# Performance work log

Hardware: AMD Instinct MI355X
Metric: run time of the kernel (lower is better)

The kernel has to match this reference:

```python
import jax, jax.numpy as jnp
import numpy as np

N, IN_F, OUT_F, R = 8192, 4096, 4096, 16
ALPHA = 32
SCALING = ALPHA / R  # 2.0


def setup_inputs() -> dict:
    key = jax.random.key(0)
    k1, k2, k3, k4, k5 = jax.random.split(key, 5)
    return {
        "x": jax.random.normal(k1, (N, IN_F), dtype=jnp.float32),
        "W": jax.random.normal(k2, (OUT_F, IN_F), dtype=jnp.float32) * 0.02,
        "b": jax.random.normal(k3, (OUT_F,), dtype=jnp.float32) * 0.02,
        "lora_A": jax.random.normal(k4, (R, IN_F), dtype=jnp.float32) * 0.02,
        "lora_B": jax.random.normal(k5, (OUT_F, R), dtype=jnp.float32) * 0.02,
    }


def reference(x, W, b, lora_A, lora_B):
    # Base linear: x [N, in_f] @ W.T [in_f, out_f] + b -> [N, out_f]
    result = jnp.einsum('ni,oi->no', x, W) + b
    # LoRA path: (B @ (A @ x.T)).T * scaling == (x @ A.T) @ B.T * scaling
    lora = jnp.einsum('nr,or->no', jnp.einsum('ni,ri->nr', x, lora_A), lora_B)
    return result + lora * SCALING
```

## Files before the change

kernel.cpp:

```cpp
#include <hip/hip_runtime.h>
#include <hip/hip_bf16.h>
#include <stdint.h>

#define N_ROWS 8192
#define IN_F   4096
#define OUT_F  4096
#define R_LORA 16
#define KP     4160

typedef __bf16 bf16_t;
typedef __attribute__((ext_vector_type(8))) __bf16 bf16x8;
typedef __attribute__((ext_vector_type(4))) __bf16 bf16x4;
typedef __attribute__((ext_vector_type(4))) float  f32x4;
typedef __attribute__((ext_vector_type(16))) float f32x16;

__device__ __forceinline__ void load16_lds(const bf16_t* g, bf16_t* l) {
    auto gp = (const __attribute__((address_space(1))) void*)g;
    auto lp = (__attribute__((address_space(3))) void*)(uint32_t)(uintptr_t)l;
    __builtin_amdgcn_global_load_lds(gp, lp, 16, 0, 0);
}

#define PREPA_BLOCKS 2048

__global__ __launch_bounds__(256) void prep_fused(const float* __restrict__ x,
                                                  const float* __restrict__ W,
                                                  const float* __restrict__ bias,
                                                  const float* __restrict__ lA,
                                                  const float* __restrict__ lB,
                                                  bf16_t* __restrict__ Aw,
                                                  bf16_t* __restrict__ Bw) {
    int b = blockIdx.x;
    int t = threadIdx.x;
    if (b < PREPA_BLOCKS) {
        int row0 = b * 4;
        for (int rr = 0; rr < 4; ++rr) {
            int row = row0 + rr;
            const float4* xr = (const float4*)(x + (size_t)row * IN_F);
            bf16_t* ar = Aw + (size_t)row * KP;
            for (int s = t; s < 512; s += 256) {
                float4 f0 = xr[2 * s];
                float4 f1 = xr[2 * s + 1];
                bf16x8 v;
                v[0] = (bf16_t)f0.x; v[1] = (bf16_t)f0.y;
                v[2] = (bf16_t)f0.z; v[3] = (bf16_t)f0.w;
                v[4] = (bf16_t)f1.x; v[5] = (bf16_t)f1.y;
                v[6] = (bf16_t)f1.z; v[7] = (bf16_t)f1.w;
                *(bf16x8*)(ar + s * 8) = v;
            }
            if (t < 64) ar[IN_F + t] = (t == 0) ? (bf16_t)1.0f : (bf16_t)0.0f;
        }
    } else {
        int o0 = (b - PREPA_BLOCKS) * 4;
        float bl[4][R_LORA];
        for (int oo = 0; oo < 4; ++oo)
            for (int r = 0; r < R_LORA; ++r)
                bl[oo][r] = 2.0f * lB[(o0 + oo) * R_LORA + r];

        for (int j = 0; j < IN_F / (256 * 4); ++j) {
            int i4 = (j * 256 + t) * 4;
            f32x4 acc[4];
            for (int oo = 0; oo < 4; ++oo) {
                float4 w = *(const float4*)(W + (size_t)(o0 + oo) * IN_F + i4);
                acc[oo] = (f32x4){w.x, w.y, w.z, w.w};
            }
            for (int r = 0; r < R_LORA; ++r) {
                float4 a = *(const float4*)(lA + (size_t)r * IN_F + i4);
                for (int oo = 0; oo < 4; ++oo) {
                    acc[oo][0] += bl[oo][r] * a.x;
                    acc[oo][1] += bl[oo][r] * a.y;
                    acc[oo][2] += bl[oo][r] * a.z;
                    acc[oo][3] += bl[oo][r] * a.w;
                }
            }
            for (int oo = 0; oo < 4; ++oo) {
                bf16x4 v;
                v[0] = (bf16_t)acc[oo][0]; v[1] = (bf16_t)acc[oo][1];
                v[2] = (bf16_t)acc[oo][2]; v[3] = (bf16_t)acc[oo][3];
                *(bf16x4*)(Bw + (size_t)(o0 + oo) * KP + i4) = v;
            }
        }
        {
            int oo = t >> 6;
            int c  = IN_F + (t & 63);
            float v = (c == IN_F) ? bias[o0 + oo] : 0.0f;
            Bw[(size_t)(o0 + oo) * KP + c] = (bf16_t)v;
        }
    }
}

#define BM 256
#define BN 256
#define BK 64
#define NT (KP / BK)

__global__ __launch_bounds__(512, 2) void gemm_bt(const bf16_t* __restrict__ A,
                                                  const bf16_t* __restrict__ B,
                                                  float* __restrict__ C) {
    __shared__ __align__(16) bf16_t lds[2][2][BM * BK];

    int bid = blockIdx.x;
    int swz = (bid & 7) * 64 + (bid >> 3);
    int bm  = swz & 31;
    int bn  = swz >> 5;
    int rowBase = bm * BM;
    int colBase = bn * BN;

    const int t    = threadIdx.x;
    const int lane = t & 63;
    const int wave = t >> 6;
    const int l31  = lane & 31;
    const int lhi  = lane >> 5;
    const int l7   = lane & 7;
    const int lsw  = l7 ^ (2 * (l31 >> 3));
    const int wr   = wave >> 2;
    const int wc   = wave & 3;

    int rowOffA[4], colOffB[2];
#pragma unroll
    for (int rf = 0; rf < 4; ++rf) rowOffA[rf] = (wr * 128 + rf * 32 + l31) * BK;
#pragma unroll
    for (int cf = 0; cf < 2; ++cf) colOffB[cf] = (wc * 64 + cf * 32 + l31) * BK;

    uint32_t srcA[4], srcB[4];
#pragma unroll
    for (int s = 0; s < 4; ++s) {
        int c = s * 512 + t;
        int r = c >> 3, p = c & 7;
        int ck = p ^ (r & 7) ^ (2 * ((r >> 3) & 3));
        uint32_t off = (uint32_t)(r * KP + (ck << 3));
        srcA[s] = (uint32_t)(rowBase * KP) + off;
        srcB[s] = (uint32_t)(colBase * KP) + off;
    }

    auto stage = [&](int bsel, int k0) {
#pragma unroll
        for (int s = 0; s < 4; ++s)
            load16_lds(A + srcA[s] + k0, &lds[bsel][0][(s * 512 + t) * 8]);
#pragma unroll
        for (int s = 0; s < 4; ++s)
            load16_lds(B + srcB[s] + k0, &lds[bsel][1][(s * 512 + t) * 8]);
    };

    f32x16 acc[4][2];
#pragma unroll
    for (int rf = 0; rf < 4; ++rf)
#pragma unroll
        for (int cf = 0; cf < 2; ++cf)
#pragma unroll
            for (int r = 0; r < 16; ++r) acc[rf][cf][r] = 0.f;

#define COMPUTE(bsel)                                                          \
    do {                                                                       \
        const bf16_t* Ab = &lds[bsel][0][0];                                   \
        const bf16_t* Bb = &lds[bsel][1][0];                                   \
        _Pragma("unroll")                                                      \
        for (int ks = 0; ks < 4; ++ks) {                                       \
            int pos = ((((ks << 1) | lhi)) ^ lsw) << 3;                        \
            bf16x8 af[4], bf[2];                                               \
            _Pragma("unroll")                                                  \
            for (int rf = 0; rf < 4; ++rf)                                     \
                af[rf] = *(const bf16x8*)&Ab[rowOffA[rf] + pos];               \
            _Pragma("unroll")                                                  \
            for (int cf = 0; cf < 2; ++cf)                                     \
                bf[cf] = *(const bf16x8*)&Bb[colOffB[cf] + pos];               \
            __builtin_amdgcn_s_setprio(1);                                     \
            _Pragma("unroll")                                                  \
            for (int rf = 0; rf < 4; ++rf)                                     \
                _Pragma("unroll")                                              \
                for (int cf = 0; cf < 2; ++cf)                                 \
                    acc[rf][cf] = __builtin_amdgcn_mfma_f32_32x32x16_bf16(     \
                        af[rf], bf[cf], acc[rf][cf], 0, 0, 0);                 \
            __builtin_amdgcn_s_setprio(0);                                     \
        }                                                                      \
    } while (0)

    stage(0, 0);

    for (int kt = 0; kt < NT - 1; ++kt) {
        const int cur = kt & 1;
        const int nb  = cur ^ 1;
        __builtin_amdgcn_s_barrier();
        stage(nb, (kt + 1) * BK);
        asm volatile("s_waitcnt vmcnt(8)" ::: "memory");
        __builtin_amdgcn_s_barrier();
        COMPUTE(cur);
    }
    {
        __builtin_amdgcn_s_barrier();
        asm volatile("s_waitcnt vmcnt(0)" ::: "memory");
        __builtin_amdgcn_s_barrier();
        COMPUTE(0);
    }
#undef COMPUTE

#pragma unroll
    for (int rf = 0; rf < 4; ++rf) {
        int rB = rowBase + wr * 128 + rf * 32 + 4 * lhi;
#pragma unroll
        for (int cf = 0; cf < 2; ++cf) {
            int col = colBase + wc * 64 + cf * 32 + l31;
#pragma unroll
            for (int reg = 0; reg < 16; ++reg) {
                int row = rB + (reg & 3) + 8 * (reg >> 2);
                C[(size_t)row * OUT_F + col] = acc[rf][cf][reg];
            }
        }
    }
}

extern "C" void kernel_launch(void* const* d_in, const int* in_sizes, int n_in,
                              void* d_out, int out_size, void* d_ws, size_t ws_size,
                              hipStream_t stream) {
    const float* x  = (const float*)d_in[0];
    const float* W  = (const float*)d_in[1];
    const float* b  = (const float*)d_in[2];
    const float* lA = (const float*)d_in[3];
    const float* lB = (const float*)d_in[4];
    float* out = (float*)d_out;

    bf16_t* Aw = (bf16_t*)d_ws;
    bf16_t* Bw = Aw + (size_t)N_ROWS * KP;

    prep_fused<<<PREPA_BLOCKS + OUT_F / 4, 256, 0, stream>>>(x, W, b, lA, lB, Aw, Bw);
    gemm_bt<<<(N_ROWS / BM) * (OUT_F / BN), 512, 0, stream>>>(Aw, Bw, out);
}
```

Before: 542.7 us.

## Split GEMM main loop into four quadrant phases interleaving loads with MFMA

Restructures each wave's output tile into four quadrants spread across the block tile, and splits each k-step into four phases. Each phase reads A/B fragments from LDS, issues half of the next tile's global-to-LDS loads, and runs MFMAs on one quadrant, with explicit waitcnts, barriers and sched_barriers between phases. The aim is to overlap LDS reads and global prefetch with matrix-core work, in the style of ping-pong scheduling. The cost is more barriers and tighter dependence on exact vmcnt/lgkmcnt bookkeeping. The epilogue store mapping changes to match the new quadrant layout.

```diff
diff --git a/kernel.cpp b/kernel.cpp
--- a/kernel.cpp
+++ b/kernel.cpp
@@ -115,11 +115,18 @@
     const int wr   = wave >> 2;
     const int wc   = wave & 3;
 
-    int rowOffA[4], colOffB[2];
-#pragma unroll
-    for (int rf = 0; rf < 4; ++rf) rowOffA[rf] = (wr * 128 + rf * 32 + l31) * BK;
-#pragma unroll
-    for (int cf = 0; cf < 2; ++cf) colOffB[cf] = (wc * 64 + cf * 32 + l31) * BK;
+    int rowA_[2][2], colB_[2];
+#pragma unroll
+    for (int qa = 0; qa < 2; ++qa)
+#pragma unroll
+        for (int i = 0; i < 2; ++i)
+            rowA_[qa][i] = (qa * 128 + wr * 64 + i * 32 + l31) * BK;
+#pragma unroll
+    for (int qb = 0; qb < 2; ++qb)
+        colB_[qb] = (qb * 128 + wc * 32 + l31) * BK;
+    int pos_[4];
+#pragma unroll
+    for (int ks = 0; ks < 4; ++ks) pos_[ks] = ((((ks << 1) | lhi)) ^ lsw) << 3;
 
     uint32_t srcA[4], srcB[4];
 #pragma unroll
@@ -132,77 +139,144 @@
         srcB[s] = (uint32_t)(colBase * KP) + off;
     }
 
-    auto stage = [&](int bsel, int k0) {
-#pragma unroll
-        for (int s = 0; s < 4; ++s)
+    auto stage2A = [&](int bsel, int k0, int half) {
+#pragma unroll
+        for (int s2 = 0; s2 < 2; ++s2) {
+            int s = half * 2 + s2;
             load16_lds(A + srcA[s] + k0, &lds[bsel][0][(s * 512 + t) * 8]);
-#pragma unroll
-        for (int s = 0; s < 4; ++s)
+        }
+    };
+    auto stage2B = [&](int bsel, int k0, int half) {
+#pragma unroll
+        for (int s2 = 0; s2 < 2; ++s2) {
+            int s = half * 2 + s2;
             load16_lds(B + srcB[s] + k0, &lds[bsel][1][(s * 512 + t) * 8]);
+        }
     };
 
     f32x16 acc[4][2];
 #pragma unroll
-    for (int rf = 0; rf < 4; ++rf)
-#pragma unroll
-        for (int cf = 0; cf < 2; ++cf)
-#pragma unroll
-            for (int r = 0; r < 16; ++r) acc[rf][cf][r] = 0.f;
-
-#define COMPUTE(bsel)                                                          \
+    for (int q = 0; q < 4; ++q)
+#pragma unroll
+        for (int i = 0; i < 2; ++i)
+#pragma unroll
+            for (int r = 0; r < 16; ++r) acc[q][i][r] = 0.f;
+
+    bf16x8 af[2][4];
+    bf16x8 bfr[4];
+
+#define RD_A(qa_)                                                              \
     do {                                                                       \
-        const bf16_t* Ab = &lds[bsel][0][0];                                   \
-        const bf16_t* Bb = &lds[bsel][1][0];                                   \
         _Pragma("unroll")                                                      \
-        for (int ks = 0; ks < 4; ++ks) {                                       \
-            int pos = ((((ks << 1) | lhi)) ^ lsw) << 3;                        \
-            bf16x8 af[4], bf[2];                                               \
+        for (int i = 0; i < 2; ++i)                                            \
             _Pragma("unroll")                                                  \
-            for (int rf = 0; rf < 4; ++rf)                                     \
-                af[rf] = *(const bf16x8*)&Ab[rowOffA[rf] + pos];               \
+            for (int ks = 0; ks < 4; ++ks)                                     \
+                af[i][ks] = *(const bf16x8*)&Ab[rowA_[qa_][i] + pos_[ks]];     \
+    } while (0)
+
+#define RD_B(qb_)                                                              \
+    do {                                                                       \
+        _Pragma("unroll")                                                      \
+        for (int ks = 0; ks < 4; ++ks)                                         \
+            bfr[ks] = *(const bf16x8*)&Bb[colB_[qb_] + pos_[ks]];              \
+    } while (0)
+
+#define MMA_Q(q_)                                                              \
+    do {                                                                       \
+        asm volatile("s_waitcnt lgkmcnt(0)" ::: "memory");                     \
+        __builtin_amdgcn_sched_barrier(0);                                     \
+        __builtin_amdgcn_s_setprio(1);                                         \
+        _Pragma("unroll")                                                      \
+        for (int ks = 0; ks < 4; ++ks)                                         \
             _Pragma("unroll")                                                  \
-            for (int cf = 0; cf < 2; ++cf)                                     \
-                bf[cf] = *(const bf16x8*)&Bb[colOffB[cf] + pos];               \
-            __builtin_amdgcn_s_setprio(1);                                     \
-            _Pragma("unroll")                                                  \
-            for (int rf = 0; rf < 4; ++rf)                                     \
-                _Pragma("unroll")                                              \
-                for (int cf = 0; cf < 2; ++cf)                                 \
-                    acc[rf][cf] = __builtin_amdgcn_mfma_f32_32x32x16_bf16(     \
-                        af[rf], bf[cf], acc[rf][cf], 0, 0, 0);                 \
-            __builtin_amdgcn_s_setprio(0);                                     \
-        }                                                                      \
+            for (int i = 0; i < 2; ++i)                                        \
+                acc[q_][i] = __builtin_amdgcn_mfma_f32_32x32x16_bf16(          \
+                    af[i][ks], bfr[ks], acc[q_][i], 0, 0, 0);                  \
+        __builtin_amdgcn_s_setprio(0);                                         \
     } while (0)
 
-    stage(0, 0);
+#define SBAR __builtin_amdgcn_s_barrier()
+#define PIN  __builtin_amdgcn_sched_barrier(0)
+
+    stage2A(0, 0, 0);
+    stage2B(0, 0, 0);
+    stage2A(0, 0, 1);
+    stage2B(0, 0, 1);
+    asm volatile("s_waitcnt vmcnt(4)" ::: "memory");
+    SBAR;
 
     for (int kt = 0; kt < NT - 1; ++kt) {
         const int cur = kt & 1;
         const int nb  = cur ^ 1;
-        __builtin_amdgcn_s_barrier();
-        stage(nb, (kt + 1) * BK);
-        asm volatile("s_waitcnt vmcnt(8)" ::: "memory");
-        __builtin_amdgcn_s_barrier();
-        COMPUTE(cur);
+        const int k1  = (kt + 1) * BK;
+        const bf16_t* Ab = &lds[cur][0][0];
+        const bf16_t* Bb = &lds[cur][1][0];
+
+        RD_A(0); RD_B(0);
+        stage2A(nb, k1, 0);
+        asm volatile("s_waitcnt lgkmcnt(8)" ::: "memory");
+        PIN; SBAR;
+        MMA_Q(0);
+        asm volatile("s_waitcnt vmcnt(4)" ::: "memory");
+        SBAR;
+        RD_A(1);
+        stage2B(nb, k1, 0);
+        PIN; SBAR;
+        MMA_Q(1);
+        asm volatile("s_waitcnt vmcnt(4)" ::: "memory");
+        SBAR;
+        RD_B(1);
+        stage2A(nb, k1, 1);
+        PIN; SBAR;
+        MMA_Q(2);
+        SBAR;
+        RD_A(0);
+        stage2B(nb, k1, 1);
+        PIN; SBAR;
+        MMA_Q(3);
+        asm volatile("s_waitcnt vmcnt(4)" ::: "memory");
+        SBAR;
     }
     {
-        __builtin_amdgcn_s_barrier();
+        const bf16_t* Ab = &lds[0][0][0];
+        const bf16_t* Bb = &lds[0][1][0];
+        RD_A(0); RD_B(0);
+        asm volatile("s_waitcnt lgkmcnt(8)" ::: "memory");
+        PIN; SBAR;
+        MMA_Q(0);
+        asm volatile("s_waitcnt vmcnt(2)" ::: "memory");
+        SBAR;
+        RD_A(1);
+        PIN; SBAR;
+        MMA_Q(1);
         asm volatile("s_waitcnt vmcnt(0)" ::: "memory");
-        __builtin_amdgcn_s_barrier();
-        COMPUTE(0);
-    }
-#undef COMPUTE
-
-#pragma unroll
-    for (int rf = 0; rf < 4; ++rf) {
-        int rB = rowBase + wr * 128 + rf * 32 + 4 * lhi;
-#pragma unroll
-        for (int cf = 0; cf < 2; ++cf) {
-            int col = colBase + wc * 64 + cf * 32 + l31;
+        SBAR;
+        RD_B(1);
+        PIN; SBAR;
+        MMA_Q(2);
+        SBAR;
+        RD_A(0);
+        PIN; SBAR;
+        MMA_Q(3);
+    }
+#undef RD_A
+#undef RD_B
+#undef MMA_Q
+#undef SBAR
+#undef PIN
+
+    const int qa_[4] = {0, 1, 1, 0};
+    const int qb_[4] = {0, 0, 1, 1};
+#pragma unroll
+    for (int q = 0; q < 4; ++q) {
+#pragma unroll
+        for (int i = 0; i < 2; ++i) {
+            int rB  = rowBase + qa_[q] * 128 + wr * 64 + i * 32 + 4 * lhi;
+            int col = colBase + qb_[q] * 128 + wc * 32 + l31;
 #pragma unroll
             for (int reg = 0; reg < 16; ++reg) {
                 int row = rB + (reg & 3) + 8 * (reg >> 2);
-                C[(size_t)row * OUT_F + col] = acc[rf][cf][reg];
+                C[(size_t)row * OUT_F + col] = acc[q][i][reg];
             }
         }
     }
```

New measurement: 549.8 us. No clear change (+1.3%).
